# Performance work log

Measured on AMD Instinct MI355X. Metric: run time of the kernel, lower is better.

The kernel has to match this reference:

```python
import jax, jax.numpy as jnp
import numpy as np

N_NODES = 100000
FEAT = 256
HID = 256
BATCH = 512
NUM_SAMPLES = [25, 10]  # layer_infos[0].num_samples, layer_infos[1].num_samples


def setup_inputs() -> dict:
    key = jax.random.key(0)
    ks = jax.random.split(key, 7)
    scale = 0.05
    return {
        "features": jax.random.normal(ks[0], (N_NODES, FEAT), dtype=jnp.float32),
        "adj": jax.random.randint(ks[1], (N_NODES, NUM_SAMPLES[0]), 0, N_NODES, dtype=jnp.int32),
        "batch": jax.random.randint(ks[2], (BATCH,), 0, N_NODES, dtype=jnp.int32),
        "W_self_0": jax.random.normal(ks[3], (FEAT, HID), dtype=jnp.float32) * scale,
        "W_neigh_0": jax.random.normal(ks[4], (FEAT, HID), dtype=jnp.float32) * scale,
        "W_self_1": jax.random.normal(ks[5], (HID, HID), dtype=jnp.float32) * scale,
        "W_neigh_1": jax.random.normal(ks[6], (HID, HID), dtype=jnp.float32) * scale,
    }


def reference(features, adj, batch, W_self_0, W_neigh_0, W_self_1, W_neigh_1):
    B = batch.shape[0]
    n_layers = 2
    # --- sample(): reverse-order neighbor expansion (deterministic: first-k slots) ---
    # hop 1 uses layer_infos[-1].num_samples = 10, hop 2 uses layer_infos[0].num_samples = 25
    s1 = adj[batch][:, : NUM_SAMPLES[1]].reshape(-1)  # [B*10]
    s2 = adj[s1][:, : NUM_SAMPLES[0]].reshape(-1)     # [B*250]
    support = [1, NUM_SAMPLES[1], NUM_SAMPLES[1] * NUM_SAMPLES[0]]  # [1, 10, 250]
    # --- gather input features per hop (irregular gather, memory bound) ---
    hidden = [features[batch], features[s1], features[s2]]
    Ws = [(W_self_0, W_neigh_0), (W_self_1, W_neigh_1)]
    for layer in range(n_layers):
        act = jax.nn.relu if layer < n_layers - 1 else (lambda x: x)
        W_s, W_n = Ws[layer]
        next_hidden = []
        for hop in range(n_layers - layer):
            n_smp = NUM_SAMPLES[n_layers - hop - 1]
            self_vecs = hidden[hop]  # [B*support[hop], d]
            neigh = hidden[hop + 1].reshape(B * support[hop], n_smp, -1)
            neigh_mean = neigh.mean(axis=1)  # mean aggregator
            # concat=False -> sum of self and neighbor transforms
            next_hidden.append(act(self_vecs @ W_s + neigh_mean @ W_n))
        hidden = next_hidden
    out = hidden[0]  # [B, HID]
    # GraphSAGE l2-normalizes final embeddings
    norm = jnp.maximum(jnp.linalg.norm(out, axis=1, keepdims=True), 1e-12)
    return out / norm
```

## Files before the change

kernel.cpp:

```cpp
#include <hip/hip_runtime.h>
#include <cstdint>
#include <cstddef>

#define NNODES 100000
#define FEATD  256
#define HIDD   256
#define NBATCH 512
#define FAN1   10
#define FAN2   25
#define NS1    (NBATCH*FAN1)
#define MTOT   (NBATCH+NS1)

typedef __attribute__((ext_vector_type(8))) short short8;
typedef __attribute__((ext_vector_type(4))) float f32x4;

__device__ __forceinline__ unsigned short f2bf(float f) {
    unsigned int u = __float_as_uint(f);
    unsigned int r = (u + 0x7fffu + ((u >> 16) & 1u)) >> 16;
    return (unsigned short)r;
}
__device__ __forceinline__ float bf2f(unsigned short h) {
    return __uint_as_float(((unsigned int)h) << 16);
}

template<int FAN>
__device__ __forceinline__ float4 neigh_mean(
    const float* __restrict__ feat, const int* __restrict__ arow, int l) {
    static_assert(FAN % 5 == 0, "FAN must be a multiple of 5");
    int myidx = (l < FAN) ? arow[l] : 0;
    float4 c0, c1, c2, c3, c4, n0, n1, n2, n3, n4;
#define GLD(K) (*reinterpret_cast<const float4*>( \
        feat + (size_t)__shfl(myidx, (K)) * FEATD + l * 4))
    c0 = GLD(0); c1 = GLD(1); c2 = GLD(2); c3 = GLD(3); c4 = GLD(4);
    float4 a = make_float4(0.f, 0.f, 0.f, 0.f);
    constexpr int NB = FAN / 5;
    #pragma unroll
    for (int g = 0; g < NB; ++g) {
        if (g + 1 < NB) {
            n0 = GLD(5*g+5); n1 = GLD(5*g+6); n2 = GLD(5*g+7);
            n3 = GLD(5*g+8); n4 = GLD(5*g+9);
        }
        a.x += (c0.x + c1.x) + (c2.x + c3.x) + c4.x;
        a.y += (c0.y + c1.y) + (c2.y + c3.y) + c4.y;
        a.z += (c0.z + c1.z) + (c2.z + c3.z) + c4.z;
        a.w += (c0.w + c1.w) + (c2.w + c3.w) + c4.w;
        if (g + 1 < NB) { c0 = n0; c1 = n1; c2 = n2; c3 = n3; c4 = n4; }
    }
#undef GLD
    const float s = 1.0f / (float)FAN;
    a.x *= s; a.y *= s; a.z *= s; a.w *= s;
    return a;
}

__global__ __launch_bounds__(256) void k_wcvt(
    const float* __restrict__ Ws0, const float* __restrict__ Wn0,
    const float* __restrict__ Ws1, const float* __restrict__ Wn1,
    unsigned short* __restrict__ B0t, unsigned short* __restrict__ B1t) {
    __shared__ unsigned short Ts[64][72];
    const int t     = threadIdx.x;
    const int which = blockIdx.x >> 5;
    const int loc   = blockIdx.x & 31;
    const int kt = loc >> 2, nt = loc & 3;
    const int k0 = kt * 64, n0 = nt * 64;
    const float* W;
    if (which == 0)
        W = (k0 < 256) ? (Ws0 + (size_t)k0 * 256) : (Wn0 + (size_t)(k0 - 256) * 256);
    else
        W = (k0 < 256) ? (Ws1 + (size_t)k0 * 256) : (Wn1 + (size_t)(k0 - 256) * 256);
    unsigned short* Bt = which ? B1t : B0t;
    #pragma unroll
    for (int i = 0; i < 4; ++i) {
        int s  = t + i * 256;
        int kr = s >> 4;
        int c4 = s & 15;
        float4 v = *reinterpret_cast<const float4*>(W + (size_t)kr * 256 + n0 + c4 * 4);
        Ts[c4 * 4 + 0][kr] = f2bf(v.x);
        Ts[c4 * 4 + 1][kr] = f2bf(v.y);
        Ts[c4 * 4 + 2][kr] = f2bf(v.z);
        Ts[c4 * 4 + 3][kr] = f2bf(v.w);
    }
    __syncthreads();
    #pragma unroll
    for (int i = 0; i < 2; ++i) {
        int s  = t + i * 256;
        int nl = s >> 3;
        int k8 = (s & 7) * 8;
        *reinterpret_cast<short8*>(Bt + (size_t)(n0 + nl) * 512 + k0 + k8) =
            *reinterpret_cast<const short8*>(&Ts[nl][k8]);
    }
}

__global__ __launch_bounds__(256) void k_gg0(
    const float* __restrict__ feat, const int* __restrict__ adj,
    const int* __restrict__ batch, const unsigned short* __restrict__ B0t,
    unsigned short* __restrict__ H0, unsigned short* __restrict__ H1) {
    __shared__ __align__(16) unsigned short As[16][520];
    const int t   = threadIdx.x;
    const int wv  = t >> 6;
    const int l   = t & 63;
    const int q   = l >> 4;
    const int m15 = l & 15;
    const int r0  = blockIdx.x * 16;
    const bool isBatch = (r0 < NBATCH);

    #pragma unroll
    for (int i = 0; i < 4; ++i) {
        const int r = wv * 4 + i;
        const int R = r0 + r;
        int node;
        if (isBatch) {
            node = batch[R];
        } else {
            int idx = R - NBATCH;
            int b   = idx / FAN1;
            int j   = idx - b * FAN1;
            node = adj[(size_t)batch[b] * FAN2 + j];
        }
        float4 selfv = *reinterpret_cast<const float4*>(
            feat + (size_t)node * FEATD + l * 4);
        const int* arow = adj + (size_t)node * FAN2;
        float4 mean = isBatch ? neigh_mean<FAN1>(feat, arow, l)
                              : neigh_mean<FAN2>(feat, arow, l);
        ushort4 ps, pn;
        ps.x = f2bf(selfv.x); ps.y = f2bf(selfv.y);
        ps.z = f2bf(selfv.z); ps.w = f2bf(selfv.w);
        pn.x = f2bf(mean.x);  pn.y = f2bf(mean.y);
        pn.z = f2bf(mean.z);  pn.w = f2bf(mean.w);
        *reinterpret_cast<ushort4*>(&As[r][l * 4])       = ps;
        *reinterpret_cast<ushort4*>(&As[r][256 + l * 4]) = pn;
    }
    __syncthreads();

    f32x4 acc0 = (f32x4)0.f, acc1 = (f32x4)0.f, acc2 = (f32x4)0.f, acc3 = (f32x4)0.f;
    const unsigned short* b0p = B0t + (size_t)(wv * 64 +  0 + m15) * 512;
    const unsigned short* b1p = B0t + (size_t)(wv * 64 + 16 + m15) * 512;
    const unsigned short* b2p = B0t + (size_t)(wv * 64 + 32 + m15) * 512;
    const unsigned short* b3p = B0t + (size_t)(wv * 64 + 48 + m15) * 512;
    #pragma unroll
    for (int kt = 0; kt < 16; ++kt) {
        const int kk = kt * 32 + q * 8;
        short8 a  = *reinterpret_cast<const short8*>(&As[m15][kk]);
        short8 b0 = *reinterpret_cast<const short8*>(b0p + kk);
        short8 b1 = *reinterpret_cast<const short8*>(b1p + kk);
        short8 b2 = *reinterpret_cast<const short8*>(b2p + kk);
        short8 b3 = *reinterpret_cast<const short8*>(b3p + kk);
        acc0 = __builtin_amdgcn_mfma_f32_16x16x32_bf16(a, b0, acc0, 0, 0, 0);
        acc1 = __builtin_amdgcn_mfma_f32_16x16x32_bf16(a, b1, acc1, 0, 0, 0);
        acc2 = __builtin_amdgcn_mfma_f32_16x16x32_bf16(a, b2, acc2, 0, 0, 0);
        acc3 = __builtin_amdgcn_mfma_f32_16x16x32_bf16(a, b3, acc3, 0, 0, 0);
    }

    #pragma unroll
    for (int f = 0; f < 4; ++f) {
        const int n = wv * 64 + f * 16 + m15;
        const f32x4& a = (f == 0) ? acc0 : (f == 1) ? acc1 : (f == 2) ? acc2 : acc3;
        #pragma unroll
        for (int j = 0; j < 4; ++j) {
            int m = r0 + q * 4 + j;
            unsigned short v = f2bf(fmaxf(a[j], 0.f));
            if (isBatch)
                H0[(size_t)m * HIDD + n] = v;
            else
                H1[(size_t)(m - NBATCH) * HIDD + n] = v;
        }
    }
}

__global__ __launch_bounds__(512) void k_l1(
    const unsigned short* __restrict__ H0, const unsigned short* __restrict__ H1,
    const unsigned short* __restrict__ B1t, float* __restrict__ out) {
    __shared__ __align__(16) unsigned short As[16][520];
    __shared__ float rn[16][8];
    const int t   = threadIdx.x;
    const int wv  = t >> 6;
    const int l   = t & 63;
    const int q   = l >> 4;
    const int m15 = l & 15;
    const int rb  = blockIdx.x * 16;

    {
        int r = t >> 5, c8 = (t & 31) * 8;
        *reinterpret_cast<short8*>(&As[r][c8]) =
            *reinterpret_cast<const short8*>(H0 + (size_t)(rb + r) * HIDD + c8);
    }
    {
        int r = t >> 5, c8 = (t & 31) * 8;
        const unsigned short* base = H1 + (size_t)(rb + r) * FAN1 * HIDD + c8;
        float a[8];
        #pragma unroll
        for (int e = 0; e < 8; ++e) a[e] = 0.f;
        #pragma unroll
        for (int j = 0; j < FAN1; ++j) {
            short8 v = *reinterpret_cast<const short8*>(base + (size_t)j * HIDD);
            #pragma unroll
            for (int e = 0; e < 8; ++e) a[e] += bf2f((unsigned short)v[e]);
        }
        short8 p;
        #pragma unroll
        for (int e = 0; e < 8; ++e) p[e] = (short)f2bf(a[e] * (1.0f / FAN1));
        *reinterpret_cast<short8*>(&As[r][256 + c8]) = p;
    }
    __syncthreads();

    f32x4 acc0 = (f32x4)0.f, acc1 = (f32x4)0.f;
    const unsigned short* b0p = B1t + (size_t)(wv * 32 + m15) * 512;
    const unsigned short* b1p = B1t + (size_t)(wv * 32 + 16 + m15) * 512;
    #pragma unroll
    for (int kt = 0; kt < 8; ++kt) {
        const int kb = kt * 64;
        #pragma unroll
        for (int s2 = 0; s2 < 2; ++s2) {
            const int kk = kb + s2 * 32 + q * 8;
            short8 a  = *reinterpret_cast<const short8*>(&As[m15][kk]);
            short8 b0 = *reinterpret_cast<const short8*>(b0p + kk);
            short8 b1 = *reinterpret_cast<const short8*>(b1p + kk);
            acc0 = __builtin_amdgcn_mfma_f32_16x16x32_bf16(a, b0, acc0, 0, 0, 0);
            acc1 = __builtin_amdgcn_mfma_f32_16x16x32_bf16(a, b1, acc1, 0, 0, 0);
        }
    }

    #pragma unroll
    for (int j = 0; j < 4; ++j) {
        float p = acc0[j] * acc0[j] + acc1[j] * acc1[j];
        p += __shfl_xor(p, 1);
        p += __shfl_xor(p, 2);
        p += __shfl_xor(p, 4);
        p += __shfl_xor(p, 8);
        if (m15 == 0) rn[q * 4 + j][wv] = p;
    }
    __syncthreads();

    #pragma unroll
    for (int j = 0; j < 4; ++j) {
        const int m = q * 4 + j;
        float s = rn[m][0] + rn[m][1] + rn[m][2] + rn[m][3]
                + rn[m][4] + rn[m][5] + rn[m][6] + rn[m][7];
        float inv = 1.0f / fmaxf(sqrtf(s), 1e-12f);
        out[(size_t)(rb + m) * HIDD + wv * 32 + m15]      = acc0[j] * inv;
        out[(size_t)(rb + m) * HIDD + wv * 32 + 16 + m15] = acc1[j] * inv;
    }
}

extern "C" void kernel_launch(void* const* d_in, const int* in_sizes, int n_in,
                              void* d_out, int out_size, void* d_ws, size_t ws_size,
                              hipStream_t stream) {
    const float* feat  = (const float*)d_in[0];
    const int*   adj   = (const int*)d_in[1];
    const int*   batch = (const int*)d_in[2];
    const float* Ws0   = (const float*)d_in[3];
    const float* Wn0   = (const float*)d_in[4];
    const float* Ws1   = (const float*)d_in[5];
    const float* Wn1   = (const float*)d_in[6];
    float* out = (float*)d_out;

    char* ws = (char*)d_ws;
    unsigned short* B0t = (unsigned short*)(ws + 0);
    unsigned short* B1t = (unsigned short*)(ws + 262144);
    unsigned short* H0  = (unsigned short*)(ws + 524288);
    unsigned short* H1  = (unsigned short*)(ws + 786432);

    k_wcvt<<<64, 256, 0, stream>>>(Ws0, Wn0, Ws1, Wn1, B0t, B1t);
    k_gg0<<<MTOT / 16, 256, 0, stream>>>(feat, adj, batch, B0t, H0, H1);
    k_l1<<<NBATCH / 16, 512, 0, stream>>>(H0, H1, B1t, out);
}
```

Baseline: 193.4 us.

## Precompute sampled index lists and batch four-row gathers for memory-level parallelism

Adds a prep kernel, merged with the weight conversion, that resolves the hop-1 and hop-2 sample index lists (s1, s2) into workspace. The gather kernel then loads all four rows' index vectors up front and streams their neighbor loads through one software-pipelined loop instead of four serial dependent chains. The aim is to remove dependent adj lookups from the gather critical path and keep more loads in flight per wave. In exchange it adds an extra global round trip for the index arrays and raises register pressure.

```diff
diff --git a/kernel.cpp b/kernel.cpp
--- a/kernel.cpp
+++ b/kernel.cpp
@@ -23,76 +23,113 @@
     return __uint_as_float(((unsigned int)h) << 16);
 }
 
+__global__ __launch_bounds__(256) void k_prep(
+    const float* __restrict__ Ws0, const float* __restrict__ Wn0,
+    const float* __restrict__ Ws1, const float* __restrict__ Wn1,
+    const int* __restrict__ adj, const int* __restrict__ batch,
+    unsigned short* __restrict__ B0t, unsigned short* __restrict__ B1t,
+    int* __restrict__ s1, int* __restrict__ s2) {
+    const int t = threadIdx.x;
+    if (blockIdx.x < 64) {
+        __shared__ unsigned short Ts[64][72];
+        const int which = blockIdx.x >> 5;
+        const int loc   = blockIdx.x & 31;
+        const int kt = loc >> 2, nt = loc & 3;
+        const int k0 = kt * 64, n0 = nt * 64;
+        const float* W;
+        if (which == 0)
+            W = (k0 < 256) ? (Ws0 + (size_t)k0 * 256) : (Wn0 + (size_t)(k0 - 256) * 256);
+        else
+            W = (k0 < 256) ? (Ws1 + (size_t)k0 * 256) : (Wn1 + (size_t)(k0 - 256) * 256);
+        unsigned short* Bt = which ? B1t : B0t;
+        #pragma unroll
+        for (int i = 0; i < 4; ++i) {
+            int s  = t + i * 256;
+            int kr = s >> 4;
+            int c4 = s & 15;
+            float4 v = *reinterpret_cast<const float4*>(W + (size_t)kr * 256 + n0 + c4 * 4);
+            Ts[c4 * 4 + 0][kr] = f2bf(v.x);
+            Ts[c4 * 4 + 1][kr] = f2bf(v.y);
+            Ts[c4 * 4 + 2][kr] = f2bf(v.z);
+            Ts[c4 * 4 + 3][kr] = f2bf(v.w);
+        }
+        __syncthreads();
+        #pragma unroll
+        for (int i = 0; i < 2; ++i) {
+            int s  = t + i * 256;
+            int nl = s >> 3;
+            int k8 = (s & 7) * 8;
+            *reinterpret_cast<short8*>(Bt + (size_t)(n0 + nl) * 512 + k0 + k8) =
+                *reinterpret_cast<const short8*>(&Ts[nl][k8]);
+        }
+        return;
+    }
+    __shared__ int hs[FAN1];
+    const int b  = blockIdx.x - 64;
+    const int nb = batch[b];
+    if (t < FAN1) {
+        int v = adj[(size_t)nb * FAN2 + t];
+        s1[b * FAN1 + t] = v;
+        hs[t] = v;
+    }
+    __syncthreads();
+    if (t < FAN1 * FAN2) {
+        const int u = t / FAN2, v = t - u * FAN2;
+        s2[(size_t)(b * FAN1 + u) * FAN2 + v] = adj[(size_t)hs[u] * FAN2 + v];
+    }
+}
+
 template<int FAN>
-__device__ __forceinline__ float4 neigh_mean(
-    const float* __restrict__ feat, const int* __restrict__ arow, int l) {
+__device__ __forceinline__ void gather4(
+    const float* __restrict__ feat, const int* nidx, const int* node,
+    int l, int wv, unsigned short (*As)[520]) {
     static_assert(FAN % 5 == 0, "FAN must be a multiple of 5");
-    int myidx = (l < FAN) ? arow[l] : 0;
+    constexpr int BPR = FAN / 5;
+    constexpr int NB4 = 4 * BPR;
+    float4 sv0 = *reinterpret_cast<const float4*>(feat + (size_t)node[0] * FEATD + l * 4);
+    float4 sv1 = *reinterpret_cast<const float4*>(feat + (size_t)node[1] * FEATD + l * 4);
+    float4 sv2 = *reinterpret_cast<const float4*>(feat + (size_t)node[2] * FEATD + l * 4);
+    float4 sv3 = *reinterpret_cast<const float4*>(feat + (size_t)node[3] * FEATD + l * 4);
+#define GLD(ROW, K) (*reinterpret_cast<const float4*>( \
+        feat + (size_t)__shfl(nidx[ROW], (K)) * FEATD + l * 4))
     float4 c0, c1, c2, c3, c4, n0, n1, n2, n3, n4;
-#define GLD(K) (*reinterpret_cast<const float4*>( \
-        feat + (size_t)__shfl(myidx, (K)) * FEATD + l * 4))
-    c0 = GLD(0); c1 = GLD(1); c2 = GLD(2); c3 = GLD(3); c4 = GLD(4);
+    c0 = GLD(0, 0); c1 = GLD(0, 1); c2 = GLD(0, 2); c3 = GLD(0, 3); c4 = GLD(0, 4);
     float4 a = make_float4(0.f, 0.f, 0.f, 0.f);
-    constexpr int NB = FAN / 5;
-    #pragma unroll
-    for (int g = 0; g < NB; ++g) {
-        if (g + 1 < NB) {
-            n0 = GLD(5*g+5); n1 = GLD(5*g+6); n2 = GLD(5*g+7);
-            n3 = GLD(5*g+8); n4 = GLD(5*g+9);
+    #pragma unroll
+    for (int g = 0; g < NB4; ++g) {
+        const int row = g / BPR;
+        if (g + 1 < NB4) {
+            const int nr = (g + 1) / BPR;
+            const int nk = ((g + 1) % BPR) * 5;
+            n0 = GLD(nr, nk + 0); n1 = GLD(nr, nk + 1); n2 = GLD(nr, nk + 2);
+            n3 = GLD(nr, nk + 3); n4 = GLD(nr, nk + 4);
         }
         a.x += (c0.x + c1.x) + (c2.x + c3.x) + c4.x;
         a.y += (c0.y + c1.y) + (c2.y + c3.y) + c4.y;
         a.z += (c0.z + c1.z) + (c2.z + c3.z) + c4.z;
         a.w += (c0.w + c1.w) + (c2.w + c3.w) + c4.w;
-        if (g + 1 < NB) { c0 = n0; c1 = n1; c2 = n2; c3 = n3; c4 = n4; }
+        if ((g + 1) % BPR == 0) {
+            const float s = 1.0f / (float)FAN;
+            float4 sv = (row == 0) ? sv0 : (row == 1) ? sv1 : (row == 2) ? sv2 : sv3;
+            ushort4 ps, pn;
+            ps.x = f2bf(sv.x);      ps.y = f2bf(sv.y);
+            ps.z = f2bf(sv.z);      ps.w = f2bf(sv.w);
+            pn.x = f2bf(a.x * s);   pn.y = f2bf(a.y * s);
+            pn.z = f2bf(a.z * s);   pn.w = f2bf(a.w * s);
+            const int r = wv * 4 + row;
+            *reinterpret_cast<ushort4*>(&As[r][l * 4])       = ps;
+            *reinterpret_cast<ushort4*>(&As[r][256 + l * 4]) = pn;
+            a = make_float4(0.f, 0.f, 0.f, 0.f);
+        }
+        if (g + 1 < NB4) { c0 = n0; c1 = n1; c2 = n2; c3 = n3; c4 = n4; }
     }
 #undef GLD
-    const float s = 1.0f / (float)FAN;
-    a.x *= s; a.y *= s; a.z *= s; a.w *= s;
-    return a;
-}
-
-__global__ __launch_bounds__(256) void k_wcvt(
-    const float* __restrict__ Ws0, const float* __restrict__ Wn0,
-    const float* __restrict__ Ws1, const float* __restrict__ Wn1,
-    unsigned short* __restrict__ B0t, unsigned short* __restrict__ B1t) {
-    __shared__ unsigned short Ts[64][72];
-    const int t     = threadIdx.x;
-    const int which = blockIdx.x >> 5;
-    const int loc   = blockIdx.x & 31;
-    const int kt = loc >> 2, nt = loc & 3;
-    const int k0 = kt * 64, n0 = nt * 64;
-    const float* W;
-    if (which == 0)
-        W = (k0 < 256) ? (Ws0 + (size_t)k0 * 256) : (Wn0 + (size_t)(k0 - 256) * 256);
-    else
-        W = (k0 < 256) ? (Ws1 + (size_t)k0 * 256) : (Wn1 + (size_t)(k0 - 256) * 256);
-    unsigned short* Bt = which ? B1t : B0t;
-    #pragma unroll
-    for (int i = 0; i < 4; ++i) {
-        int s  = t + i * 256;
-        int kr = s >> 4;
-        int c4 = s & 15;
-        float4 v = *reinterpret_cast<const float4*>(W + (size_t)kr * 256 + n0 + c4 * 4);
-        Ts[c4 * 4 + 0][kr] = f2bf(v.x);
-        Ts[c4 * 4 + 1][kr] = f2bf(v.y);
-        Ts[c4 * 4 + 2][kr] = f2bf(v.z);
-        Ts[c4 * 4 + 3][kr] = f2bf(v.w);
-    }
-    __syncthreads();
-    #pragma unroll
-    for (int i = 0; i < 2; ++i) {
-        int s  = t + i * 256;
-        int nl = s >> 3;
-        int k8 = (s & 7) * 8;
-        *reinterpret_cast<short8*>(Bt + (size_t)(n0 + nl) * 512 + k0 + k8) =
-            *reinterpret_cast<const short8*>(&Ts[nl][k8]);
-    }
 }
 
 __global__ __launch_bounds__(256) void k_gg0(
-    const float* __restrict__ feat, const int* __restrict__ adj,
-    const int* __restrict__ batch, const unsigned short* __restrict__ B0t,
+    const float* __restrict__ feat, const int* __restrict__ batch,
+    const int* __restrict__ s1, const int* __restrict__ s2,
+    const unsigned short* __restrict__ B0t,
     unsigned short* __restrict__ H0, unsigned short* __restrict__ H1) {
     __shared__ __align__(16) unsigned short As[16][520];
     const int t   = threadIdx.x;
@@ -103,32 +140,21 @@
     const int r0  = blockIdx.x * 16;
     const bool isBatch = (r0 < NBATCH);
 
+    int node[4], nidx[4];
     #pragma unroll
     for (int i = 0; i < 4; ++i) {
-        const int r = wv * 4 + i;
-        const int R = r0 + r;
-        int node;
+        const int R = r0 + wv * 4 + i;
         if (isBatch) {
-            node = batch[R];
+            node[i] = batch[R];
+            nidx[i] = (l < FAN1) ? s1[R * FAN1 + l] : 0;
         } else {
-            int idx = R - NBATCH;
-            int b   = idx / FAN1;
-            int j   = idx - b * FAN1;
-            node = adj[(size_t)batch[b] * FAN2 + j];
-        }
-        float4 selfv = *reinterpret_cast<const float4*>(
-            feat + (size_t)node * FEATD + l * 4);
-        const int* arow = adj + (size_t)node * FAN2;
-        float4 mean = isBatch ? neigh_mean<FAN1>(feat, arow, l)
-                              : neigh_mean<FAN2>(feat, arow, l);
-        ushort4 ps, pn;
-        ps.x = f2bf(selfv.x); ps.y = f2bf(selfv.y);
-        ps.z = f2bf(selfv.z); ps.w = f2bf(selfv.w);
-        pn.x = f2bf(mean.x);  pn.y = f2bf(mean.y);
-        pn.z = f2bf(mean.z);  pn.w = f2bf(mean.w);
-        *reinterpret_cast<ushort4*>(&As[r][l * 4])       = ps;
-        *reinterpret_cast<ushort4*>(&As[r][256 + l * 4]) = pn;
-    }
+            const int idx = R - NBATCH;
+            node[i] = s1[idx];
+            nidx[i] = (l < FAN2) ? s2[(size_t)idx * FAN2 + l] : 0;
+        }
+    }
+    if (isBatch) gather4<FAN1>(feat, nidx, node, l, wv, As);
+    else         gather4<FAN2>(feat, nidx, node, l, wv, As);
     __syncthreads();
 
     f32x4 acc0 = (f32x4)0.f, acc1 = (f32x4)0.f, acc2 = (f32x4)0.f, acc3 = (f32x4)0.f;
@@ -209,8 +235,8 @@
     for (int kt = 0; kt < 8; ++kt) {
         const int kb = kt * 64;
         #pragma unroll
-        for (int s2 = 0; s2 < 2; ++s2) {
-            const int kk = kb + s2 * 32 + q * 8;
+        for (int s2i = 0; s2i < 2; ++s2i) {
+            const int kk = kb + s2i * 32 + q * 8;
             short8 a  = *reinterpret_cast<const short8*>(&As[m15][kk]);
             short8 b0 = *reinterpret_cast<const short8*>(b0p + kk);
             short8 b1 = *reinterpret_cast<const short8*>(b1p + kk);
@@ -258,8 +284,11 @@
     unsigned short* B1t = (unsigned short*)(ws + 262144);
     unsigned short* H0  = (unsigned short*)(ws + 524288);
     unsigned short* H1  = (unsigned short*)(ws + 786432);
-
-    k_wcvt<<<64, 256, 0, stream>>>(Ws0, Wn0, Ws1, Wn1, B0t, B1t);
-    k_gg0<<<MTOT / 16, 256, 0, stream>>>(feat, adj, batch, B0t, H0, H1);
+    int*            s1  = (int*)(ws + 3407872);
+    int*            s2  = (int*)(ws + 3428352);
+
+    k_prep<<<64 + NBATCH, 256, 0, stream>>>(Ws0, Wn0, Ws1, Wn1, adj, batch,
+                                            B0t, B1t, s1, s2);
+    k_gg0<<<MTOT / 16, 256, 0, stream>>>(feat, batch, s1, s2, B0t, H0, H1);
     k_l1<<<NBATCH / 16, 512, 0, stream>>>(H0, H1, B1t, out);
 }
```

New measurement: 193.0 us. About the same (-0.2%).
